# Optimization experiments

Hardware: AMD Instinct MI355X
Metric: run time of the kernel (lower is better)

## Reference

```python
import jax, jax.numpy as jnp
import numpy as np

# 5x5 neighborhood offsets as (dx, dy), row-major as in the original delta list
DELTA = [(dx, dy) for dy in (-2, -1, 0, 1, 2) for dx in (-2, -1, 0, 1, 2)]
BN_EPS = 1e-5


def _conv(x, w, padding):
    return jax.lax.conv_general_dilated(
        x, w, window_strides=(1, 1), padding=padding,
        dimension_numbers=('NCHW', 'OIHW', 'NCHW'))


def setup_inputs() -> dict:
    key = jax.random.key(0)
    ks = jax.random.split(key, 4)
    B, C, H, W = 128, 256, 24, 24
    source_feature = jax.random.normal(ks[0], (B, C, H, W), jnp.float32)
    detection_feature = jax.random.normal(ks[1], (B, C, H, W), jnp.float32)
    w1 = jax.random.normal(ks[2], (256, 512, 3, 3), jnp.float32) * 0.02
    b1 = jnp.zeros((256,), jnp.float32)
    bn_gamma = jnp.ones((256,), jnp.float32)
    bn_beta = jnp.zeros((256,), jnp.float32)
    bn_mean = jnp.zeros((256,), jnp.float32)
    bn_var = jnp.ones((256,), jnp.float32)
    w2 = jax.random.normal(ks[3], (25, 256, 1, 1), jnp.float32) * 0.05
    b2 = jnp.zeros((25,), jnp.float32)
    return dict(source_feature=source_feature, detection_feature=detection_feature,
                w1=w1, b1=b1, bn_gamma=bn_gamma, bn_beta=bn_beta,
                bn_mean=bn_mean, bn_var=bn_var, w2=w2, b2=b2)


def reference(source_feature, detection_feature, w1, b1, bn_gamma, bn_beta,
              bn_mean, bn_var, w2, b2):
    B, C, H, W = source_feature.shape
    # kernel_pre: Conv3x3(512->256, pad 1) + BN + ReLU + Conv1x1(256->25)
    concat_f = jnp.concatenate([source_feature, detection_feature], axis=1)  # [B,512,H,W]
    x = _conv(concat_f, w1, ((1, 1), (1, 1))) + b1[None, :, None, None]
    inv = bn_gamma / jnp.sqrt(bn_var + BN_EPS)
    x = x * inv[None, :, None, None] + (bn_beta - bn_mean * inv)[None, :, None, None]
    x = jax.nn.relu(x)
    logits = _conv(x, w2, ((0, 0), (0, 0))) + b2[None, :, None, None]  # [B,25,H,W]
    # per-pixel softmax over the 25 neighborhood taps
    kmaps = jax.nn.softmax(logits, axis=1)  # [B,25,H,W]
    # propagate: softmax-weighted 5x5 neighbor gather-sum; out-of-bounds taps
    # contribute zero (matches the skipped-boundary terms in the original loop)
    padded = jnp.pad(source_feature, ((0, 0), (0, 0), (2, 2), (2, 2)))
    prop = jnp.zeros_like(source_feature)
    for order, (dx, dy) in enumerate(DELTA):
        shifted = padded[:, :, 2 + dy:2 + dy + H, 2 + dx:2 + dx + W]  # [B,C,H,W]
        prop = prop + shifted * kmaps[:, order][:, None]  # broadcast over C
    return prop
```

## Files before the change

### kernel.cpp

```cpp
#include <hip/hip_runtime.h>
#include <hip/hip_bf16.h>
#include <stdint.h>

#define BATCH 128
#define CIN   256
#define CCAT  512
#define HH    24
#define WW    24
#define HP    26
#define WP    26
#define COUT  256
#define KDIM  4608
#define NPIX  576
#define MDIM  73728
#define NORD  25

typedef __attribute__((ext_vector_type(8))) short bf16x8;
typedef __attribute__((ext_vector_type(4))) float f32x4;

__device__ __forceinline__ unsigned short f2bf(float v) {
    union { float f; unsigned u; } x; x.f = v;
    unsigned r = x.u + 0x7fffu + ((x.u >> 16) & 1u);
    return (unsigned short)(r >> 16);
}
__device__ __forceinline__ float bf_lo(unsigned w) {
    union { unsigned u; float f; } x; x.u = w << 16; return x.f;
}
__device__ __forceinline__ float bf_hi(unsigned w) {
    union { unsigned u; float f; } x; x.u = w & 0xffff0000u; return x.f;
}

__device__ __forceinline__ void async_copy16(const void* gsrc, void* ldst) {
    __builtin_amdgcn_global_load_lds(
        (const __attribute__((address_space(1))) unsigned int*)gsrc,
        (__attribute__((address_space(3))) unsigned int*)ldst, 16, 0, 0);
}

#define PTILE 192
#define LSTR  72
__global__ __launch_bounds__(256) void prep_transpose(
        const float* __restrict__ src, const float* __restrict__ det,
        unsigned short* __restrict__ apad) {
    __shared__ unsigned short lds[PTILE * LSTR];
    int pt = blockIdx.x;
    int cg = blockIdx.y;
    int b  = blockIdx.z;
    int c0 = cg * 64;
    int p0 = pt * PTILE;
    const float* inp = (c0 < CIN)
        ? (src + ((long)b * CIN + c0) * NPIX)
        : (det + ((long)b * CIN + (c0 - CIN)) * NPIX);
    int tid = threadIdx.x;

    #pragma unroll
    for (int it = 0; it < 12; it++) {
        int l  = it * 256 + tid;
        int cq = l / PTILE;
        int px = l - cq * PTILE;
        const float* pb = inp + (long)cq * 4 * NPIX + p0 + px;
        unsigned short v0 = f2bf(pb[0 * NPIX]);
        unsigned short v1 = f2bf(pb[1 * NPIX]);
        unsigned short v2 = f2bf(pb[2 * NPIX]);
        unsigned short v3 = f2bf(pb[3 * NPIX]);
        uint2 w;
        w.x = (unsigned)v0 | ((unsigned)v1 << 16);
        w.y = (unsigned)v2 | ((unsigned)v3 << 16);
        *(uint2*)&lds[px * LSTR + cq * 4] = w;
    }
    __syncthreads();

    #pragma unroll
    for (int it = 0; it < 6; it++) {
        int l   = it * 256 + tid;
        int px  = l >> 3;
        int ch8 = l & 7;
        uint4 w = *(const uint4*)&lds[px * LSTR + ch8 * 8];
        int p  = p0 + px;
        int y  = p / WW, x = p - y * WW;
        long o = (((long)b * HP + (y + 1)) * WP + (x + 1)) * CCAT + c0 + ch8 * 8;
        *(uint4*)(apad + o) = w;
    }
}

__global__ __launch_bounds__(256) void zero_halo(unsigned short* __restrict__ apad) {
    int t = blockIdx.x * 256 + threadIdx.x;
    int ch8 = t & 63;
    int r   = t >> 6;
    int hp  = r % 100;
    int b   = r / 100;
    int y, x;
    if (hp < 26)      { y = 0;       x = hp; }
    else if (hp < 52) { y = 25;      x = hp - 26; }
    else if (hp < 76) { y = hp - 51; x = 0; }
    else              { y = hp - 75; x = 25; }
    long o = (((long)b * HP + y) * WP + x) * CCAT + ch8 * 8;
    *(uint4*)(apad + o) = (uint4){0u, 0u, 0u, 0u};
}

__global__ __launch_bounds__(256) void prep_w(
        const float* __restrict__ w1, const float* __restrict__ b1,
        const float* __restrict__ gam, const float* __restrict__ bet,
        const float* __restrict__ mu, const float* __restrict__ var,
        unsigned short* __restrict__ bt,
        float* __restrict__ scale, float* __restrict__ shift) {
    int idx = blockIdx.x * 256 + threadIdx.x;
    if (idx < COUT * KDIM) {
        int n = idx / KDIM;
        int k = idx - n * KDIM;
        int s = k >> 9;
        int ci = k & 511;
        int ky = s / 3, kx = s - ky * 3;
        float v = w1[(((long)n * 512 + ci) * 3 + ky) * 3 + kx];
        bt[idx] = f2bf(v);
    }
    if (blockIdx.x == 0 && threadIdx.x < COUT) {
        int c = threadIdx.x;
        float inv = gam[c] * rsqrtf(var[c] + 1e-5f);
        scale[c] = inv;
        shift[c] = (b1[c] - mu[c]) * inv + bet[c];
    }
}

#define ABUF_SH 12288
#define BUF_SH  20480
#define STAGE_A(j, nb, soff) \
    async_copy16(apad + aSrc[j] + (soff), (void*)&lds[(nb)*BUF_SH + (j)*4096 + w*512])
#define STAGE_B(j, nb, koff) \
    async_copy16(bt + bSrc[j] + (koff), (void*)&lds[(nb)*BUF_SH + ABUF_SH + (j)*4096 + w*512])
#define BAR()  __builtin_amdgcn_s_barrier()
#define WAITV2() { asm volatile("s_waitcnt vmcnt(2)" ::: "memory"); }
#define WAITV0() { asm volatile("s_waitcnt vmcnt(0)" ::: "memory"); }
#define WAITL()  { asm volatile("s_waitcnt lgkmcnt(0)" ::: "memory"); __builtin_amdgcn_sched_barrier(0); }

#define AFRAGS(csw) { \
    _Pragma("unroll") \
    for (int m = 0; m < 3; m++) \
        afr[m] = *(const bf16x8*)(L + aBase + m * 2048 + (csw)); }
#define BFRAGS(csw) { \
    _Pragma("unroll") \
    for (int n = 0; n < 4; n++) \
        bfr[n] = *(const bf16x8*)(L + bBase + n * 2048 + (csw)); }
#define DOMFMA() { \
    __builtin_amdgcn_s_setprio(1); \
    _Pragma("unroll") \
    for (int m = 0; m < 3; m++) \
        _Pragma("unroll") \
        for (int n = 0; n < 4; n++) \
            acc[m][n] = __builtin_amdgcn_mfma_f32_16x16x32_bf16( \
                afr[m], bfr[n], acc[m][n], 0, 0, 0); \
    __builtin_amdgcn_s_setprio(0); }

__global__ __launch_bounds__(512, 2) void conv1_gemm(
        const unsigned short* __restrict__ apad,
        const unsigned short* __restrict__ bt,
        const float* __restrict__ scale, const float* __restrict__ shift,
        unsigned short* __restrict__ xout) {
    __shared__ unsigned short lds[2 * BUF_SH];
    const int tid  = threadIdx.x;
    const int w    = tid >> 6;
    const int lane = tid & 63;
    const int wr = w >> 1, wc = w & 1;
    const int fr = lane & 15, ls = lane >> 4;

    const int Lb = blockIdx.x;
    const int logical = (Lb & 7) * 96 + (Lb >> 3);
    const int n0 = (logical & 1) * 128;
    const long m0 = (long)(logical >> 1) * 192;

    const int rowq = tid >> 3;
    const int sl   = (tid & 7) ^ (rowq & 7);
    long aSrc[3], bSrc[2];
    #pragma unroll
    for (int j = 0; j < 3; j++) {
        int r = j * 64 + rowq;
        long m = m0 + r;
        int b  = (int)(m / NPIX);
        int rr = (int)(m - (long)b * NPIX);
        int y = rr / WW, x = rr - y * WW;
        aSrc[j] = (((long)b * HP + y) * WP + x) * (long)CCAT + sl * 8;
    }
    #pragma unroll
    for (int j = 0; j < 2; j++)
        bSrc[j] = (long)(n0 + j * 64 + rowq) * KDIM + sl * 8;

    const int rb   = fr & 7;
    const int csw0 = ((ls    ) ^ rb) << 4;
    const int csw1 = ((ls + 4) ^ rb) << 4;
    const int aBase = (wr * 48 + fr) * 128;
    const int bBase = 24576 + (wc * 64 + fr) * 128;

    f32x4 acc[3][4];
    #pragma unroll
    for (int i = 0; i < 3; i++)
        #pragma unroll
        for (int j = 0; j < 4; j++) acc[i][j] = (f32x4){0.f, 0.f, 0.f, 0.f};

    STAGE_B(0, 0, 0); STAGE_B(1, 0, 0);
    STAGE_A(0, 0, 0); STAGE_A(1, 0, 0); STAGE_A(2, 0, 0);

    bf16x8 afr[3], bfr[4];
    int nb = 0;
    for (int kt = 0; kt < 71; kt++) {
        const int ktn = kt + 1;
        const int seg = ktn >> 3;
        const int ky = seg / 3, kx = seg - ky * 3;
        const long soff = (long)(ky * WP + kx) * CCAT + (ktn & 7) * 64;
        const long koff = (long)ktn * 64;
        const int pb = nb ^ 1;
        const char* L = (const char*)lds + nb * (BUF_SH * 2);

        STAGE_B(0, pb, koff); STAGE_B(1, pb, koff);
        WAITV2();
        BAR();
        BFRAGS(csw0); AFRAGS(csw0);
        WAITL();
        DOMFMA();

        BFRAGS(csw1); AFRAGS(csw1);
        STAGE_A(0, pb, soff); STAGE_A(1, pb, soff); STAGE_A(2, pb, soff);
        WAITL();
        DOMFMA();
        BAR();

        nb ^= 1;
    }

    {
        const char* L = (const char*)lds + nb * (BUF_SH * 2);
        WAITV0();
        BAR();
        BFRAGS(csw0); AFRAGS(csw0); WAITL(); DOMFMA();
        BFRAGS(csw1); AFRAGS(csw1); WAITL(); DOMFMA();
    }

    #pragma unroll
    for (int n = 0; n < 4; n++) {
        int col = n0 + wc * 64 + n * 16 + fr;
        float sc = scale[col], sh = shift[col];
        #pragma unroll
        for (int m = 0; m < 3; m++) {
            long rbase = m0 + wr * 48 + m * 16 + ls * 4;
            #pragma unroll
            for (int j = 0; j < 4; j++) {
                float v = acc[m][n][j] * sc + sh;
                v = v > 0.f ? v : 0.f;
                xout[(rbase + j) * COUT + col] = f2bf(v);
            }
        }
    }
}

__global__ __launch_bounds__(256) void conv2_softmax(
        const unsigned short* __restrict__ x, const float* __restrict__ w2,
        const float* __restrict__ b2, float* __restrict__ kmaps) {
    __shared__ float w2s[NORD * 256];
    __shared__ float b2s[NORD];
    for (int i = threadIdx.x; i < NORD * 256; i += 256) w2s[i] = w2[i];
    if (threadIdx.x < NORD) b2s[threadIdx.x] = b2[threadIdx.x];
    __syncthreads();
    long pix = (long)blockIdx.x * 256 + threadIdx.x;
    float acc[NORD];
    #pragma unroll
    for (int o = 0; o < NORD; o++) acc[o] = b2s[o];
    const unsigned short* xr = x + pix * COUT;
    for (int kc = 0; kc < 32; kc++) {
        uint4 raw = *(const uint4*)(xr + kc * 8);
        float xf[8];
        xf[0] = bf_lo(raw.x); xf[1] = bf_hi(raw.x);
        xf[2] = bf_lo(raw.y); xf[3] = bf_hi(raw.y);
        xf[4] = bf_lo(raw.z); xf[5] = bf_hi(raw.z);
        xf[6] = bf_lo(raw.w); xf[7] = bf_hi(raw.w);
        #pragma unroll
        for (int o = 0; o < NORD; o++) {
            const float* wrow = &w2s[o * 256 + kc * 8];
            float4 wa = *(const float4*)(wrow);
            float4 wb = *(const float4*)(wrow + 4);
            acc[o] += xf[0] * wa.x + xf[1] * wa.y + xf[2] * wa.z + xf[3] * wa.w
                    + xf[4] * wb.x + xf[5] * wb.y + xf[6] * wb.z + xf[7] * wb.w;
        }
    }
    float mx = acc[0];
    #pragma unroll
    for (int o = 1; o < NORD; o++) mx = fmaxf(mx, acc[o]);
    float s = 0.f;
    #pragma unroll
    for (int o = 0; o < NORD; o++) { acc[o] = expf(acc[o] - mx); s += acc[o]; }
    float inv = 1.f / s;
    #pragma unroll
    for (int o = 0; o < NORD; o++) kmaps[(long)o * MDIM + pix] = acc[o] * inv;
}

__global__ __launch_bounds__(576) void propagate(
        const float* __restrict__ src, const float* __restrict__ kmaps,
        float* __restrict__ out) {
    __shared__ float sm[4][28 * 28];
    int b  = blockIdx.y;
    int cg = blockIdx.x;
    int tid = threadIdx.x;
    int y = tid / 24, x = tid - y * 24;
    long pixg = (long)b * NPIX + tid;
    float km[NORD];
    #pragma unroll
    for (int o = 0; o < NORD; o++) km[o] = kmaps[(long)o * MDIM + pixg];
    for (int r = 0; r < 16; r++) {
        int cbase = cg * 64 + r * 4;
        __syncthreads();
        for (int t = tid; t < 4 * 784; t += 576) {
            int cp = t / 784, u = t - cp * 784;
            int yy = u / 28, xx = u - yy * 28;
            float v = 0.f;
            if (yy >= 2 && yy < 26 && xx >= 2 && xx < 26)
                v = src[((long)b * CIN + cbase + cp) * NPIX + (yy - 2) * 24 + (xx - 2)];
            sm[cp][u] = v;
        }
        __syncthreads();
        #pragma unroll
        for (int cp = 0; cp < 4; cp++) {
            float a = 0.f;
            #pragma unroll
            for (int o = 0; o < NORD; o++) {
                int dy = o / 5 - 2, dx = o % 5 - 2;
                a += km[o] * sm[cp][(y + 2 + dy) * 28 + (x + 2 + dx)];
            }
            out[((long)b * CIN + cbase + cp) * NPIX + tid] = a;
        }
    }
}

extern "C" void kernel_launch(void* const* d_in, const int* in_sizes, int n_in,
                              void* d_out, int out_size, void* d_ws, size_t ws_size,
                              hipStream_t stream) {
    const float* src = (const float*)d_in[0];
    const float* det = (const float*)d_in[1];
    const float* w1  = (const float*)d_in[2];
    const float* b1  = (const float*)d_in[3];
    const float* gam = (const float*)d_in[4];
    const float* bet = (const float*)d_in[5];
    const float* mu  = (const float*)d_in[6];
    const float* var = (const float*)d_in[7];
    const float* w2  = (const float*)d_in[8];
    const float* b2  = (const float*)d_in[9];
    float* out = (float*)d_out;

    char* ws = (char*)d_ws;
    size_t off = 0;
    unsigned short* apad = (unsigned short*)(ws + off); off += (size_t)BATCH * HP * WP * CCAT * 2;
    unsigned short* bt   = (unsigned short*)(ws + off); off += (size_t)COUT * KDIM * 2;
    unsigned short* xbuf = (unsigned short*)(ws + off); off += (size_t)MDIM * COUT * 2;
    float* kmaps = (float*)(ws + off); off += (size_t)MDIM * NORD * 4;
    float* scale = (float*)(ws + off); off += 1024;
    float* shift = (float*)(ws + off); off += 1024;

    zero_halo<<<3200, 256, 0, stream>>>(apad);
    prep_transpose<<<dim3(3, 8, BATCH), 256, 0, stream>>>(src, det, apad);
    prep_w<<<4608, 256, 0, stream>>>(w1, b1, gam, bet, mu, var, bt, scale, shift);
    conv1_gemm<<<768, 512, 0, stream>>>(apad, bt, scale, shift, xbuf);
    conv2_softmax<<<288, 256, 0, stream>>>(xbuf, w2, b2, kmaps);
    propagate<<<dim3(4, BATCH), 576, 0, stream>>>(src, kmaps, out);
}
```

Measured before the change: 361.3 us.

## Rework conv1 GEMM wave tiling and interleave LDS loads with MFMA; fuse halo zeroing

The conv1 GEMM wave layout changes from 4x2 to 2x4, so each wave now owns 96 rows by 32 columns. The explicit lgkmcnt waits are dropped, and fragment loads are double-buffered and interleaved with MFMA groups so LDS reads can overlap compute. The halo-zeroing kernel is folded into prep_w, which removes one launch. In exchange, A-fragment register pressure rises, and the correctness of the LDS ordering now depends on the compiler's inserted waits.

```diff
diff --git a/kernel.cpp b/kernel.cpp
--- a/kernel.cpp
+++ b/kernel.cpp
@@ -82,28 +82,27 @@
     }
 }
 
-__global__ __launch_bounds__(256) void zero_halo(unsigned short* __restrict__ apad) {
-    int t = blockIdx.x * 256 + threadIdx.x;
-    int ch8 = t & 63;
-    int r   = t >> 6;
-    int hp  = r % 100;
-    int b   = r / 100;
-    int y, x;
-    if (hp < 26)      { y = 0;       x = hp; }
-    else if (hp < 52) { y = 25;      x = hp - 26; }
-    else if (hp < 76) { y = hp - 51; x = 0; }
-    else              { y = hp - 75; x = 25; }
-    long o = (((long)b * HP + y) * WP + x) * CCAT + ch8 * 8;
-    *(uint4*)(apad + o) = (uint4){0u, 0u, 0u, 0u};
-}
-
 __global__ __launch_bounds__(256) void prep_w(
         const float* __restrict__ w1, const float* __restrict__ b1,
         const float* __restrict__ gam, const float* __restrict__ bet,
         const float* __restrict__ mu, const float* __restrict__ var,
         unsigned short* __restrict__ bt,
-        float* __restrict__ scale, float* __restrict__ shift) {
+        float* __restrict__ scale, float* __restrict__ shift,
+        unsigned short* __restrict__ apad) {
     int idx = blockIdx.x * 256 + threadIdx.x;
+    if (idx < 128 * 100 * 64) {
+        int ch8 = idx & 63;
+        int r   = idx >> 6;
+        int hp  = r % 100;
+        int b   = r / 100;
+        int y, x;
+        if (hp < 26)      { y = 0;       x = hp; }
+        else if (hp < 52) { y = 25;      x = hp - 26; }
+        else if (hp < 76) { y = hp - 51; x = 0; }
+        else              { y = hp - 75; x = 25; }
+        long o = (((long)b * HP + y) * WP + x) * CCAT + ch8 * 8;
+        *(uint4*)(apad + o) = (uint4){0u, 0u, 0u, 0u};
+    }
     if (idx < COUT * KDIM) {
         int n = idx / KDIM;
         int k = idx - n * KDIM;
@@ -128,26 +127,26 @@
 #define STAGE_B(j, nb, koff) \
     async_copy16(bt + bSrc[j] + (koff), (void*)&lds[(nb)*BUF_SH + ABUF_SH + (j)*4096 + w*512])
 #define BAR()  __builtin_amdgcn_s_barrier()
+#define SFEN() __builtin_amdgcn_sched_barrier(0)
 #define WAITV2() { asm volatile("s_waitcnt vmcnt(2)" ::: "memory"); }
 #define WAITV0() { asm volatile("s_waitcnt vmcnt(0)" ::: "memory"); }
-#define WAITL()  { asm volatile("s_waitcnt lgkmcnt(0)" ::: "memory"); __builtin_amdgcn_sched_barrier(0); }
-
-#define AFRAGS(csw) { \
+
+#define LD_B(dst, csw) { \
+    _Pragma("unroll") \
+    for (int n = 0; n < 2; n++) \
+        dst[n] = *(const bf16x8*)(L + bBase + n * 2048 + (csw)); }
+#define LD_A(dst, mh, csw) { \
     _Pragma("unroll") \
     for (int m = 0; m < 3; m++) \
-        afr[m] = *(const bf16x8*)(L + aBase + m * 2048 + (csw)); }
-#define BFRAGS(csw) { \
-    _Pragma("unroll") \
-    for (int n = 0; n < 4; n++) \
-        bfr[n] = *(const bf16x8*)(L + bBase + n * 2048 + (csw)); }
-#define DOMFMA() { \
+        dst[m] = *(const bf16x8*)(L + aBase + ((mh) * 3 + m) * 2048 + (csw)); }
+#define MM(af, bf, mh) { \
     __builtin_amdgcn_s_setprio(1); \
     _Pragma("unroll") \
     for (int m = 0; m < 3; m++) \
         _Pragma("unroll") \
-        for (int n = 0; n < 4; n++) \
-            acc[m][n] = __builtin_amdgcn_mfma_f32_16x16x32_bf16( \
-                afr[m], bfr[n], acc[m][n], 0, 0, 0); \
+        for (int n = 0; n < 2; n++) \
+            acc[(mh) * 3 + m][n] = __builtin_amdgcn_mfma_f32_16x16x32_bf16( \
+                af[m], bf[n], acc[(mh) * 3 + m][n], 0, 0, 0); \
     __builtin_amdgcn_s_setprio(0); }
 
 __global__ __launch_bounds__(512, 2) void conv1_gemm(
@@ -159,7 +158,7 @@
     const int tid  = threadIdx.x;
     const int w    = tid >> 6;
     const int lane = tid & 63;
-    const int wr = w >> 1, wc = w & 1;
+    const int wr = w >> 2, wc = w & 3;
     const int fr = lane & 15, ls = lane >> 4;
 
     const int Lb = blockIdx.x;
@@ -186,19 +185,19 @@
     const int rb   = fr & 7;
     const int csw0 = ((ls    ) ^ rb) << 4;
     const int csw1 = ((ls + 4) ^ rb) << 4;
-    const int aBase = (wr * 48 + fr) * 128;
-    const int bBase = 24576 + (wc * 64 + fr) * 128;
-
-    f32x4 acc[3][4];
-    #pragma unroll
-    for (int i = 0; i < 3; i++)
+    const int aBase = (wr * 96 + fr) * 128;
+    const int bBase = 24576 + (wc * 32 + fr) * 128;
+
+    f32x4 acc[6][2];
+    #pragma unroll
+    for (int i = 0; i < 6; i++)
         #pragma unroll
-        for (int j = 0; j < 4; j++) acc[i][j] = (f32x4){0.f, 0.f, 0.f, 0.f};
+        for (int j = 0; j < 2; j++) acc[i][j] = (f32x4){0.f, 0.f, 0.f, 0.f};
 
     STAGE_B(0, 0, 0); STAGE_B(1, 0, 0);
     STAGE_A(0, 0, 0); STAGE_A(1, 0, 0); STAGE_A(2, 0, 0);
 
-    bf16x8 afr[3], bfr[4];
+    bf16x8 afr0[3], afr1[3], bfr0[2], bfr1[2];
     int nb = 0;
     for (int kt = 0; kt < 71; kt++) {
         const int ktn = kt + 1;
@@ -212,16 +211,22 @@
         STAGE_B(0, pb, koff); STAGE_B(1, pb, koff);
         WAITV2();
         BAR();
-        BFRAGS(csw0); AFRAGS(csw0);
-        WAITL();
-        DOMFMA();
-
-        BFRAGS(csw1); AFRAGS(csw1);
+        SFEN();
+
+        LD_B(bfr0, csw0);
+        LD_A(afr0, 0, csw0);
+        LD_A(afr1, 1, csw0);
+        MM(afr0, bfr0, 0);
         STAGE_A(0, pb, soff); STAGE_A(1, pb, soff); STAGE_A(2, pb, soff);
-        WAITL();
-        DOMFMA();
+        LD_B(bfr1, csw1);
+        LD_A(afr0, 0, csw1);
+        MM(afr1, bfr0, 1);
+        LD_A(afr1, 1, csw1);
+        MM(afr0, bfr1, 0);
+        MM(afr1, bfr1, 1);
+
+        SFEN();
         BAR();
-
         nb ^= 1;
     }
 
@@ -229,17 +234,26 @@
         const char* L = (const char*)lds + nb * (BUF_SH * 2);
         WAITV0();
         BAR();
-        BFRAGS(csw0); AFRAGS(csw0); WAITL(); DOMFMA();
-        BFRAGS(csw1); AFRAGS(csw1); WAITL(); DOMFMA();
-    }
-
-    #pragma unroll
-    for (int n = 0; n < 4; n++) {
-        int col = n0 + wc * 64 + n * 16 + fr;
+        SFEN();
+        LD_B(bfr0, csw0);
+        LD_A(afr0, 0, csw0);
+        LD_A(afr1, 1, csw0);
+        MM(afr0, bfr0, 0);
+        LD_B(bfr1, csw1);
+        LD_A(afr0, 0, csw1);
+        MM(afr1, bfr0, 1);
+        LD_A(afr1, 1, csw1);
+        MM(afr0, bfr1, 0);
+        MM(afr1, bfr1, 1);
+    }
+
+    #pragma unroll
+    for (int n = 0; n < 2; n++) {
+        int col = n0 + wc * 32 + n * 16 + fr;
         float sc = scale[col], sh = shift[col];
         #pragma unroll
-        for (int m = 0; m < 3; m++) {
-            long rbase = m0 + wr * 48 + m * 16 + ls * 4;
+        for (int m = 0; m < 6; m++) {
+            long rbase = m0 + wr * 96 + m * 16 + ls * 4;
             #pragma unroll
             for (int j = 0; j < 4; j++) {
                 float v = acc[m][n][j] * sc + sh;
@@ -351,9 +365,8 @@
     float* scale = (float*)(ws + off); off += 1024;
     float* shift = (float*)(ws + off); off += 1024;
 
-    zero_halo<<<3200, 256, 0, stream>>>(apad);
     prep_transpose<<<dim3(3, 8, BATCH), 256, 0, stream>>>(src, det, apad);
-    prep_w<<<4608, 256, 0, stream>>>(w1, b1, gam, bet, mu, var, bt, scale, shift);
+    prep_w<<<4608, 256, 0, stream>>>(w1, b1, gam, bet, mu, var, bt, scale, shift, apad);
     conv1_gemm<<<768, 512, 0, stream>>>(apad, bt, scale, shift, xbuf);
     conv2_softmax<<<288, 256, 0, stream>>>(xbuf, w2, b2, kmaps);
     propagate<<<dim3(4, BATCH), 576, 0, stream>>>(src, kmaps, out);
```

Result: no change. 354.2 us (-2.0%).
